# Kernel optimization log

Measured on AMD Instinct MI355X. Metric: run time of the kernel, lower is better.

Reference implementation:

```python
import jax, jax.numpy as jnp
import numpy as np

GRID_SIZE = 5
SPLINE_ORDER = 3
GRID_RANGE = (-1.0, 1.0)
LAYERS = [1024, 1024, 1024]
BATCH = 8192
LN_EPS = 1e-5


def _make_grid(in_features):
    h = (GRID_RANGE[1] - GRID_RANGE[0]) / GRID_SIZE
    n = GRID_SIZE + 2 * SPLINE_ORDER + 1  # 12 knots
    g = jnp.linspace(GRID_RANGE[0] - h * SPLINE_ORDER,
                     GRID_RANGE[1] + h * SPLINE_ORDER, n, dtype=jnp.float32)
    return jnp.broadcast_to(g, (in_features, n))


def setup_inputs() -> dict:
    key = jax.random.key(0)
    ks = jax.random.split(key, 8)
    n_layers = len(LAYERS) - 1
    d_in, d_out = LAYERS[0], LAYERS[1]  # square layers -> stackable params
    coeff = GRID_SIZE + SPLINE_ORDER  # 8
    # kaiming_uniform_(nonlinearity='linear'): bound = sqrt(3) * (1/sqrt(fan_in))
    bw_bound = float(np.sqrt(3.0) / np.sqrt(d_in))
    sw_bound = float(np.sqrt(3.0) / np.sqrt(d_in * coeff))
    x = jax.random.normal(ks[0], (BATCH, d_in), dtype=jnp.float32)
    base_w = jax.random.uniform(ks[1], (n_layers, d_out, d_in), jnp.float32, -bw_bound, bw_bound)
    spline_w = jax.random.uniform(ks[2], (n_layers, d_out, d_in, coeff), jnp.float32, -sw_bound, sw_bound)
    ln_g = jnp.ones((n_layers, d_out), jnp.float32)
    ln_b = jnp.zeros((n_layers, d_out), jnp.float32)
    prelu_a = jnp.full((n_layers,), 0.25, jnp.float32)
    grid = jnp.stack([_make_grid(d_in) for _ in range(n_layers)])  # [L, in, 12]
    return {"x": x, "base_w": base_w, "spline_w": spline_w,
            "ln_g": ln_g, "ln_b": ln_b, "prelu_a": prelu_a, "grid": grid}


def _bspline_bases(x, g):
    """Cox-de Boor recursion. x: [B, in], g: [in, n_knots] -> [B, in, G+order]."""
    xu = x[..., None]  # [B, in, 1]
    bases = ((xu >= g[:, :-1]) & (xu < g[:, 1:])).astype(x.dtype)  # [B, in, 11]
    for k in range(1, SPLINE_ORDER + 1):
        left = g[:, :-(k + 1)]
        right = g[:, k:-1]
        delta = jnp.where(right == left, jnp.ones_like(right), right - left)
        bases = ((xu - left) / delta * bases[..., :-1]
                 + (g[:, k + 1:] - xu) / (g[:, k + 1:] - g[:, 1:-k]) * bases[..., 1:])
    return bases  # [B, in, 8]


def kan_forward(x, base_w, spline_w, ln_g, ln_b, prelu_a, grid):
    n_layers = base_w.shape[0]
    for i in range(n_layers):
        base_out = jnp.matmul(jax.nn.gelu(x, approximate=False), base_w[i].T)  # [B, out]
        bases = _bspline_bases(x, grid[i])  # [B, in, 8]
        spline_out = jnp.matmul(bases.reshape(x.shape[0], -1),
                                spline_w[i].reshape(spline_w.shape[1], -1).T)  # [B, out]
        h = base_out + spline_out
        mu = jnp.mean(h, axis=-1, keepdims=True)
        var = jnp.var(h, axis=-1, keepdims=True)  # biased, matches torch LayerNorm
        h = (h - mu) * jax.lax.rsqrt(var + LN_EPS) * ln_g[i] + ln_b[i]
        x = jnp.where(h >= 0, h, prelu_a[i] * h)  # PReLU (scalar slope per layer)
    return x


def reference(x, base_w, spline_w, ln_g, ln_b, prelu_a, grid):
    return kan_forward(x, base_w, spline_w, ln_g, ln_b, prelu_a, grid)
```

## Files before the change

kernel.cpp:

```cpp
#include <hip/hip_runtime.h>
#include <hip/hip_bf16.h>
#include <cstdint>
#include <cstddef>

typedef __bf16 bf16_t;
typedef __bf16 bf16x8 __attribute__((ext_vector_type(8)));
typedef __bf16 bf16x4 __attribute__((ext_vector_type(4)));
typedef float  f32x4  __attribute__((ext_vector_type(4)));

#define DIM    1024
#define NCOEF  8
#define KTOT   (DIM + DIM * NCOEF)
#define NKNOT  12
#define BATCH  8192
#define LN_EPS 1e-5f

__device__ __forceinline__ float gelu_exact(float x) {
    return 0.5f * x * (1.0f + erff(x * 0.70710678118654752440f));
}

__global__ void pack_w(const float* __restrict__ bw, const float* __restrict__ sw,
                       bf16_t* __restrict__ W) {
    int idx = blockIdx.x * 256 + threadIdx.x;
    bf16_t* wrow = W + (size_t)(idx >> 10) * KTOT;
    int j = idx & 1023;
    wrow[j] = (bf16_t)bw[idx];
    const float4* sp = (const float4*)(sw + (size_t)idx * NCOEF);
    float4 s0 = sp[0], s1 = sp[1];
    bf16x8 v;
    v[0] = (bf16_t)s0.x; v[1] = (bf16_t)s0.y; v[2] = (bf16_t)s0.z; v[3] = (bf16_t)s0.w;
    v[4] = (bf16_t)s1.x; v[5] = (bf16_t)s1.y; v[6] = (bf16_t)s1.z; v[7] = (bf16_t)s1.w;
    *(bf16x8*)(wrow + DIM + j * NCOEF) = v;
}

__global__ void prep_gelu(const float* __restrict__ x, bf16_t* __restrict__ g) {
    int idx = blockIdx.x * 256 + threadIdx.x;
    float4 v = ((const float4*)x)[idx];
    bf16x4 o;
    o[0] = (bf16_t)gelu_exact(v.x); o[1] = (bf16_t)gelu_exact(v.y);
    o[2] = (bf16_t)gelu_exact(v.z); o[3] = (bf16_t)gelu_exact(v.w);
    *(bf16x4*)(g + (size_t)idx * 4) = o;
}

__device__ __forceinline__ void gl_lds16(const void* g, void* l) {
    __builtin_amdgcn_global_load_lds(
        (const __attribute__((address_space(1))) unsigned int*)(uintptr_t)g,
        (__attribute__((address_space(3))) unsigned int*)(uintptr_t)l, 16, 0, 0);
}

__device__ __forceinline__ uint64_t pack4bf(float a, float b, float c, float d) {
    union { bf16_t h[4]; uint64_t q; } u;
    u.h[0] = (bf16_t)a; u.h[1] = (bf16_t)b; u.h[2] = (bf16_t)c; u.h[3] = (bf16_t)d;
    return u.q;
}

__device__ __forceinline__ void spline8(float x, float g0, float invh,
                                        uint64_t& lo, uint64_t& hi) {
    float u = (x - g0) * invh;
    float jf = floorf(u);
    int j = (int)jf;
    float f = u - jf;
    float f2 = f * f, f3 = f2 * f;
    float om = 1.0f - f, om2 = om * om;
    float w0 = om2 * om * (1.0f / 6.0f);
    float w3 = f3 * (1.0f / 6.0f);
    float w1 = fmaf(0.5f, f3, 2.0f / 3.0f) - f2;
    float w2 = 1.0f - w0 - w1 - w3;
    uint64_t W64 = pack4bf(w0, w1, w2, w3);
    if (!(u >= 0.0f && u < 11.0f)) W64 = 0;
    int sh = (j - 3) * 16;
    if (sh >= 0) {
        int s = sh & 63;
        uint64_t loW = W64 << s;
        uint64_t hiW = s ? (W64 >> (64 - s)) : 0ull;
        lo = (sh < 64) ? loW : 0ull;
        hi = (sh < 64) ? hiW : loW;
    } else {
        lo = W64 >> (-sh);
        hi = 0ull;
    }
}

__device__ __forceinline__ void mfma_tile(const bf16_t* __restrict__ Ar0,
                                          const bf16_t* __restrict__ Ar1,
                                          const bf16_t* __restrict__ Br0,
                                          const bf16_t* __restrict__ Br1,
                                          f32x4 (&acc)[4][4]) {
#pragma unroll
    for (int kk = 0; kk < 2; kk++) {
        const bf16_t* Ar = kk ? Ar1 : Ar0;
        const bf16_t* Br = kk ? Br1 : Br0;
        bf16x8 af[4], bfr[4];
#pragma unroll
        for (int i = 0; i < 4; i++) af[i] = *(const bf16x8*)(Ar + i * 16 * 64);
#pragma unroll
        for (int j = 0; j < 4; j++) bfr[j] = *(const bf16x8*)(Br + j * 16 * 64);
#pragma unroll
        for (int i = 0; i < 4; i++)
#pragma unroll
            for (int j = 0; j < 4; j++)
                acc[i][j] = __builtin_amdgcn_mfma_f32_16x16x32_bf16(af[i], bfr[j], acc[i][j], 0, 0, 0);
    }
}

__global__ __launch_bounds__(256) void gemm_fused(
    const float* __restrict__ Y,
    const bf16_t* __restrict__ G,
    const bf16_t* __restrict__ W,
    float* __restrict__ C,
    const float* __restrict__ gp,
    int mmask, int mshift) {
    constexpr int K = KTOT, N = DIM;
    __shared__ __align__(16) bf16_t At[64 * 64];
    __shared__ __align__(16) bf16_t Bt[256 * 64];
    const int tid = threadIdx.x;
    const int l = tid & 63;
    const int w = tid >> 6;
    const int bm = blockIdx.x & mmask, bn = blockIdx.x >> mshift;

    const float g0 = gp[0];
    const float invh = 1.0f / (gp[1] - gp[0]);

    const int lrow = tid >> 3;
    const int lchk = (tid & 7) ^ (lrow & 7);
    const bf16_t* Gg = G + (size_t)(bm * 64 + lrow) * DIM + lchk * 8;
    const bf16_t* Bg = W + (size_t)(bn * 256 + lrow) * K + lchk * 8;
    bf16_t* Al = At + tid * 8;
    bf16_t* Bl = Bt + tid * 8;

    const float* Yb = Y + (size_t)(bm * 64 + lrow) * DIM + (tid & 7);
    bf16_t* As = At + lrow * 64 + lchk * 8;

    f32x4 acc[4][4] = {};
    const int cA = (l >> 4) ^ (l & 7);
    const bf16_t* Ar0 = At + (l & 15) * 64 + cA * 8;
    const bf16_t* Ar1 = At + (l & 15) * 64 + (cA ^ 4) * 8;
    const bf16_t* Br0 = Bt + (w * 64 + (l & 15)) * 64 + cA * 8;
    const bf16_t* Br1 = Bt + (w * 64 + (l & 15)) * 64 + (cA ^ 4) * 8;

    for (int k0 = 0; k0 < DIM; k0 += 64) {
#pragma unroll
        for (int q = 0; q < 2; q++)
            gl_lds16(Gg + (size_t)q * 32 * DIM + k0, Al + q * 2048);
#pragma unroll
        for (int q = 0; q < 8; q++)
            gl_lds16(Bg + (size_t)q * 32 * K + k0, Bl + q * 2048);
        asm volatile("s_waitcnt vmcnt(0)" ::: "memory");
        __syncthreads();
        mfma_tile(Ar0, Ar1, Br0, Br1, acc);
        __syncthreads();
    }

    float ycur[2], ynext[2];
#pragma unroll
    for (int q = 0; q < 2; q++) ycur[q] = Yb[(size_t)q * 32 * DIM];

    for (int k0 = DIM; k0 < K; k0 += 64) {
        const int j0 = (k0 - DIM) >> 3;
        const bool more = (k0 + 64) < K;
        if (more) {
#pragma unroll
            for (int q = 0; q < 2; q++) ynext[q] = Yb[(size_t)q * 32 * DIM + j0 + 8];
        }
#pragma unroll
        for (int q = 0; q < 8; q++)
            gl_lds16(Bg + (size_t)q * 32 * K + k0, Bl + q * 2048);
#pragma unroll
        for (int q = 0; q < 2; q++) {
            uint64_t lo, hi;
            spline8(ycur[q], g0, invh, lo, hi);
            union { uint64_t u[2]; uint4 v; } ov;
            ov.u[0] = lo; ov.u[1] = hi;
            *(uint4*)(As + q * 32 * 64) = ov.v;
        }
        asm volatile("s_waitcnt vmcnt(0)" ::: "memory");
        __syncthreads();
        mfma_tile(Ar0, Ar1, Br0, Br1, acc);
        __syncthreads();
        if (more) {
#pragma unroll
            for (int q = 0; q < 2; q++) ycur[q] = ynext[q];
        }
    }

    const int r0 = bm * 64 + (l >> 4) * 4;
    const int c0 = bn * 256 + w * 64 + (l & 15);
#pragma unroll
    for (int i = 0; i < 4; i++)
#pragma unroll
        for (int j = 0; j < 4; j++)
#pragma unroll
            for (int r = 0; r < 4; r++)
                C[(size_t)(r0 + i * 16 + r) * N + c0 + j * 16] = acc[i][j][r];
}

__global__ void ln_mid(const float* __restrict__ h, const float* __restrict__ g_ln,
                       const float* __restrict__ b_ln, const float* __restrict__ pa,
                       float* __restrict__ y, bf16_t* __restrict__ yg) {
    const int row = blockIdx.x, tid = threadIdx.x;
    const int w = tid >> 6, l = tid & 63;
    f32x4 v = *(const f32x4*)(h + (size_t)row * DIM + tid * 4);
    float s = v[0] + v[1] + v[2] + v[3];
    float q = v[0] * v[0] + v[1] * v[1] + v[2] * v[2] + v[3] * v[3];
#pragma unroll
    for (int o = 32; o > 0; o >>= 1) { s += __shfl_xor(s, o); q += __shfl_xor(q, o); }
    __shared__ float rs[4], rq[4];
    if (l == 0) { rs[w] = s; rq[w] = q; }
    __syncthreads();
    s = rs[0] + rs[1] + rs[2] + rs[3];
    q = rq[0] + rq[1] + rq[2] + rq[3];
    float mean = s * (1.0f / DIM);
    float var = q * (1.0f / DIM) - mean * mean;
    float rstd = rsqrtf(var + LN_EPS);
    float a = pa[0];
    f32x4 o4;
    bf16x4 g4;
#pragma unroll
    for (int c = 0; c < 4; c++) {
        int col = tid * 4 + c;
        float yv = (v[c] - mean) * rstd * g_ln[col] + b_ln[col];
        yv = (yv >= 0.0f) ? yv : a * yv;
        o4[c] = yv;
        g4[c] = (bf16_t)gelu_exact(yv);
    }
    *(f32x4*)(y + (size_t)row * DIM + tid * 4) = o4;
    *(bf16x4*)(yg + (size_t)row * DIM + tid * 4) = g4;
}

__global__ void ln_out(const float* __restrict__ h, const float* __restrict__ g_ln,
                       const float* __restrict__ b_ln, const float* __restrict__ pa,
                       float* __restrict__ out) {
    const int row = blockIdx.x, tid = threadIdx.x;
    const int w = tid >> 6, l = tid & 63;
    f32x4 v = *(const f32x4*)(h + (size_t)row * DIM + tid * 4);
    float s = v[0] + v[1] + v[2] + v[3];
    float q = v[0] * v[0] + v[1] * v[1] + v[2] * v[2] + v[3] * v[3];
#pragma unroll
    for (int o = 32; o > 0; o >>= 1) { s += __shfl_xor(s, o); q += __shfl_xor(q, o); }
    __shared__ float rs[4], rq[4];
    if (l == 0) { rs[w] = s; rq[w] = q; }
    __syncthreads();
    s = rs[0] + rs[1] + rs[2] + rs[3];
    q = rq[0] + rq[1] + rq[2] + rq[3];
    float mean = s * (1.0f / DIM);
    float var = q * (1.0f / DIM) - mean * mean;
    float rstd = rsqrtf(var + LN_EPS);
    float a = pa[0];
    f32x4 o4;
#pragma unroll
    for (int c = 0; c < 4; c++) {
        int col = tid * 4 + c;
        float yv = (v[c] - mean) * rstd * g_ln[col] + b_ln[col];
        o4[c] = (yv >= 0.0f) ? yv : a * yv;
    }
    *(f32x4*)(out + (size_t)row * DIM + tid * 4) = o4;
}

extern "C" void kernel_launch(void* const* d_in, const int* in_sizes, int n_in,
                              void* d_out, int out_size, void* d_ws, size_t ws_size,
                              hipStream_t stream) {
    const float* x    = (const float*)d_in[0];
    const float* bw   = (const float*)d_in[1];
    const float* sw   = (const float*)d_in[2];
    const float* ln_g = (const float*)d_in[3];
    const float* ln_b = (const float*)d_in[4];
    const float* pa   = (const float*)d_in[5];
    const float* grid = (const float*)d_in[6];
    float* out = (float*)d_out;

    const size_t wbytes = (size_t)2 * DIM * KTOT * sizeof(bf16_t);
    int R = 8192;
    while (R > 128 && wbytes + (size_t)R * DIM * 10 > ws_size) R >>= 1;
    int mtiles = R / 64;
    int mshift = 0; while ((1 << mshift) < mtiles) mshift++;
    int mmask = mtiles - 1;

    char* wsc = (char*)d_ws;
    bf16_t* Wbuf = (bf16_t*)wsc;
    bf16_t* ygel = (bf16_t*)(wsc + wbytes);
    float*  ybuf = (float*)(wsc + wbytes + (size_t)R * DIM * 2);
    float*  hbuf = (float*)(wsc + wbytes + (size_t)R * DIM * 6);

    pack_w<<<(2 * DIM * DIM) / 256, 256, 0, stream>>>(bw, sw, Wbuf);

    const int nslab = BATCH / R;
    for (int sidx = 0; sidx < nslab; sidx++) {
        const size_t row0 = (size_t)sidx * R;
        const float* x0 = x + row0 * DIM;
        prep_gelu<<<R * DIM / 1024, 256, 0, stream>>>(x0, ygel);
        gemm_fused<<<mtiles * 4, 256, 0, stream>>>(x0, ygel, Wbuf, hbuf,
                                                   grid, mmask, mshift);
        ln_mid<<<R, 256, 0, stream>>>(hbuf, ln_g, ln_b, pa, ybuf, ygel);
        gemm_fused<<<mtiles * 4, 256, 0, stream>>>(ybuf, ygel, Wbuf + (size_t)DIM * KTOT, hbuf,
                                                   grid + DIM * NKNOT, mmask, mshift);
        ln_out<<<R, 256, 0, stream>>>(hbuf, ln_g + DIM, ln_b + DIM, pa + 1, out + row0 * DIM);
    }
}
```

Before: 544.0 us.

## Rewrite fused KAN GEMM with 256x256 tiles, split-K, and multi-stage LDS pipeline

The GEMM kernel moves from 64x256 tiles with 256 threads to 256x256 tiles with 512 threads. K is split into two halves whose partial outputs are written to separate buffers and summed inside the LayerNorm kernels. A four-stage LDS ring now prefetches B, G and the raw activations through direct global-to-LDS loads, and the spline bases are computed into LDS while the matrix ops run. It uses s_setprio and a custom block-to-tile mapping. The aim is to raise data reuse and hide memory latency, at the cost of a large LDS footprint, extra partial-sum traffic and workspace, and a fragile hand-written schedule.

```diff
diff --git a/kernel.cpp b/kernel.cpp
--- a/kernel.cpp
+++ b/kernel.cpp
@@ -11,41 +11,25 @@
 #define DIM    1024
 #define NCOEF  8
 #define KTOT   (DIM + DIM * NCOEF)
+#define KHALF  (KTOT / 2)
+#define NT     144
 #define NKNOT  12
 #define BATCH  8192
 #define LN_EPS 1e-5f
 
 __device__ __forceinline__ float gelu_exact(float x) {
     return 0.5f * x * (1.0f + erff(x * 0.70710678118654752440f));
-}
-
-__global__ void pack_w(const float* __restrict__ bw, const float* __restrict__ sw,
-                       bf16_t* __restrict__ W) {
-    int idx = blockIdx.x * 256 + threadIdx.x;
-    bf16_t* wrow = W + (size_t)(idx >> 10) * KTOT;
-    int j = idx & 1023;
-    wrow[j] = (bf16_t)bw[idx];
-    const float4* sp = (const float4*)(sw + (size_t)idx * NCOEF);
-    float4 s0 = sp[0], s1 = sp[1];
-    bf16x8 v;
-    v[0] = (bf16_t)s0.x; v[1] = (bf16_t)s0.y; v[2] = (bf16_t)s0.z; v[3] = (bf16_t)s0.w;
-    v[4] = (bf16_t)s1.x; v[5] = (bf16_t)s1.y; v[6] = (bf16_t)s1.z; v[7] = (bf16_t)s1.w;
-    *(bf16x8*)(wrow + DIM + j * NCOEF) = v;
-}
-
-__global__ void prep_gelu(const float* __restrict__ x, bf16_t* __restrict__ g) {
-    int idx = blockIdx.x * 256 + threadIdx.x;
-    float4 v = ((const float4*)x)[idx];
-    bf16x4 o;
-    o[0] = (bf16_t)gelu_exact(v.x); o[1] = (bf16_t)gelu_exact(v.y);
-    o[2] = (bf16_t)gelu_exact(v.z); o[3] = (bf16_t)gelu_exact(v.w);
-    *(bf16x4*)(g + (size_t)idx * 4) = o;
 }
 
 __device__ __forceinline__ void gl_lds16(const void* g, void* l) {
     __builtin_amdgcn_global_load_lds(
         (const __attribute__((address_space(1))) unsigned int*)(uintptr_t)g,
         (__attribute__((address_space(3))) unsigned int*)(uintptr_t)l, 16, 0, 0);
+}
+__device__ __forceinline__ void gl_lds4(const void* g, void* l) {
+    __builtin_amdgcn_global_load_lds(
+        (const __attribute__((address_space(1))) unsigned int*)(uintptr_t)g,
+        (__attribute__((address_space(3))) unsigned int*)(uintptr_t)l, 4, 0, 0);
 }
 
 __device__ __forceinline__ uint64_t pack4bf(float a, float b, float c, float d) {
@@ -81,125 +65,199 @@
     }
 }
 
-__device__ __forceinline__ void mfma_tile(const bf16_t* __restrict__ Ar0,
-                                          const bf16_t* __restrict__ Ar1,
-                                          const bf16_t* __restrict__ Br0,
-                                          const bf16_t* __restrict__ Br1,
-                                          f32x4 (&acc)[4][4]) {
-#pragma unroll
-    for (int kk = 0; kk < 2; kk++) {
-        const bf16_t* Ar = kk ? Ar1 : Ar0;
-        const bf16_t* Br = kk ? Br1 : Br0;
-        bf16x8 af[4], bfr[4];
-#pragma unroll
-        for (int i = 0; i < 4; i++) af[i] = *(const bf16x8*)(Ar + i * 16 * 64);
-#pragma unroll
-        for (int j = 0; j < 4; j++) bfr[j] = *(const bf16x8*)(Br + j * 16 * 64);
-#pragma unroll
-        for (int i = 0; i < 4; i++)
-#pragma unroll
-            for (int j = 0; j < 4; j++)
-                acc[i][j] = __builtin_amdgcn_mfma_f32_16x16x32_bf16(af[i], bfr[j], acc[i][j], 0, 0, 0);
-    }
-}
-
-__global__ __launch_bounds__(256) void gemm_fused(
+__global__ void pack_w(const float* __restrict__ bw, const float* __restrict__ sw,
+                       bf16_t* __restrict__ W) {
+    int idx = blockIdx.x * 256 + threadIdx.x;
+    bf16_t* wrow = W + (size_t)(idx >> 10) * KTOT;
+    int j = idx & 1023;
+    wrow[j] = (bf16_t)bw[idx];
+    const float4* sp = (const float4*)(sw + (size_t)idx * NCOEF);
+    float4 s0 = sp[0], s1 = sp[1];
+    bf16x8 v;
+    v[0] = (bf16_t)s0.x; v[1] = (bf16_t)s0.y; v[2] = (bf16_t)s0.z; v[3] = (bf16_t)s0.w;
+    v[4] = (bf16_t)s1.x; v[5] = (bf16_t)s1.y; v[6] = (bf16_t)s1.z; v[7] = (bf16_t)s1.w;
+    *(bf16x8*)(wrow + DIM + j * NCOEF) = v;
+}
+
+__global__ void prep_gelu(const float* __restrict__ x, bf16_t* __restrict__ g) {
+    int idx = blockIdx.x * 256 + threadIdx.x;
+    float4 v = ((const float4*)x)[idx];
+    bf16x4 o;
+    o[0] = (bf16_t)gelu_exact(v.x); o[1] = (bf16_t)gelu_exact(v.y);
+    o[2] = (bf16_t)gelu_exact(v.z); o[3] = (bf16_t)gelu_exact(v.w);
+    *(bf16x4*)(g + (size_t)idx * 4) = o;
+}
+
+
+#define STAGE_B(U, S) \
+    gl_lds16(BgA + (size_t)(U) * 32, ldsb + 32768 + (S) * 8192 + tid * 8); \
+    gl_lds16(BgB + (size_t)(U) * 32, ldsb + 32768 + (S) * 8192 + 4096 + tid * 8);
+
+#define STAGE_G(U, S) \
+    gl_lds16(GgA + (size_t)(U) * 32, ldsb + (S) * 8192 + tid * 8); \
+    gl_lds16(GgB + (size_t)(U) * 32, ldsb + (S) * 8192 + 4096 + tid * 8);
+
+#define STAGE_Y(U, S) { int jb_ = jb0 + (U) * 4; \
+    gl_lds4(YgA + jb_, ldsy + (S) * 1024 + tid); \
+    gl_lds4(YgB + jb_, ldsy + (S) * 1024 + 512 + tid); }
+
+#define COMPUTE_A(S) { \
+    float x1_ = ldsy[(S) * 1024 + tid], x2_ = ldsy[(S) * 1024 + 512 + tid]; \
+    uint64_t lo_, hi_; union { uint64_t u[2]; uint4 v; } ov_; \
+    spline8(x1_, g0, invh, lo_, hi_); ov_.u[0] = lo_; ov_.u[1] = hi_; \
+    *(uint4*)(ldsb + (S) * 8192 + tid * 8) = ov_.v; \
+    spline8(x2_, g0, invh, lo_, hi_); ov_.u[0] = lo_; ov_.u[1] = hi_; \
+    *(uint4*)(ldsb + (S) * 8192 + 4096 + tid * 8) = ov_.v; }
+
+#define RD_B(S) { const bf16_t* Bb_ = ldsb + 32768 + (S) * 8192 + bOff; \
+    b0 = *(const bf16x8*)(Bb_);        b1 = *(const bf16x8*)(Bb_ + 512); \
+    b2 = *(const bf16x8*)(Bb_ + 1024); b3 = *(const bf16x8*)(Bb_ + 1536); }
+
+#define MF_ROW(I, A_) \
+    acc[I][0] = __builtin_amdgcn_mfma_f32_16x16x32_bf16(A_, b0, acc[I][0], 0, 0, 0); \
+    acc[I][1] = __builtin_amdgcn_mfma_f32_16x16x32_bf16(A_, b1, acc[I][1], 0, 0, 0); \
+    acc[I][2] = __builtin_amdgcn_mfma_f32_16x16x32_bf16(A_, b2, acc[I][2], 0, 0, 0); \
+    acc[I][3] = __builtin_amdgcn_mfma_f32_16x16x32_bf16(A_, b3, acc[I][3], 0, 0, 0);
+
+#define MF_HALF(S, IB) { const bf16_t* Ab_ = ldsb + (S) * 8192 + aOff + (IB) * 2048; \
+    bf16x8 a0_ = *(const bf16x8*)(Ab_),        a1_ = *(const bf16x8*)(Ab_ + 512), \
+           a2_ = *(const bf16x8*)(Ab_ + 1024), a3_ = *(const bf16x8*)(Ab_ + 1536); \
+    __builtin_amdgcn_s_setprio(1); \
+    MF_ROW((IB) * 4 + 0, a0_) MF_ROW((IB) * 4 + 1, a1_) \
+    MF_ROW((IB) * 4 + 2, a2_) MF_ROW((IB) * 4 + 3, a3_) \
+    __builtin_amdgcn_s_setprio(0); }
+
+#define ITER(T, SA0, SA1, SS0, SS1) { \
+    const int u2_ = 2 * (T) + 2, u3_ = 2 * (T) + 3; \
+    bf16x8 b0, b1, b2, b3; \
+     \
+    if (u2_ < NT) { STAGE_B(u2_, SS0) } \
+    if ((T) < 70) { asm volatile("s_waitcnt vmcnt(6)" ::: "memory"); } \
+    else          { asm volatile("s_waitcnt vmcnt(0)" ::: "memory"); } \
+    __builtin_amdgcn_s_barrier(); \
+    asm volatile("" ::: "memory"); \
+    RD_B(SA0) \
+    MF_HALF(SA0, 0) \
+    __builtin_amdgcn_s_barrier(); \
+     \
+    if (u2_ + 2 < NT && (koff0 + (u2_ + 2) * 32) >= DIM) { STAGE_Y(u2_ + 2, SA0) } \
+    if (u2_ < NT) { \
+        if (koff0 + u2_ * 32 < DIM) { STAGE_G(u2_, SS0) } \
+        else                        { COMPUTE_A(SS0) } \
+    } \
+    MF_HALF(SA0, 1) \
+     \
+    if (u3_ < NT) { STAGE_B(u3_, SS1) } \
+    if ((T) < 70) { asm volatile("s_waitcnt vmcnt(6)" ::: "memory"); } \
+    else          { asm volatile("s_waitcnt vmcnt(0)" ::: "memory"); } \
+    __builtin_amdgcn_s_barrier(); \
+    asm volatile("" ::: "memory"); \
+    RD_B(SA1) \
+    MF_HALF(SA1, 0) \
+    __builtin_amdgcn_s_barrier(); \
+     \
+    if (u3_ + 2 < NT && (koff0 + (u3_ + 2) * 32) >= DIM) { STAGE_Y(u3_ + 2, SA1) } \
+    if (u3_ < NT) { \
+        if (koff0 + u3_ * 32 < DIM) { STAGE_G(u3_, SS1) } \
+        else                        { COMPUTE_A(SS1) } \
+    } \
+    MF_HALF(SA1, 1) \
+    asm volatile("s_waitcnt lgkmcnt(0)" ::: "memory"); \
+    __builtin_amdgcn_s_barrier(); \
+}
+
+__global__ __launch_bounds__(512, 2) void gemm_fused(
     const float* __restrict__ Y,
     const bf16_t* __restrict__ G,
     const bf16_t* __restrict__ W,
     float* __restrict__ C,
     const float* __restrict__ gp,
-    int mmask, int mshift) {
-    constexpr int K = KTOT, N = DIM;
-    __shared__ __align__(16) bf16_t At[64 * 64];
-    __shared__ __align__(16) bf16_t Bt[256 * 64];
+    int mmask, int mshift, int rows) {
+    __shared__ __align__(16) unsigned char smem[147456];
+    bf16_t* __restrict__ ldsb = (bf16_t*)smem;
+    float*  __restrict__ ldsy = (float*)(smem + 131072);
+
     const int tid = threadIdx.x;
-    const int l = tid & 63;
-    const int w = tid >> 6;
-    const int bm = blockIdx.x & mmask, bn = blockIdx.x >> mshift;
+    const int l = tid & 63, wv = tid >> 6;
+    const int wm = wv >> 2, wn = wv & 3;
+
+    const int chunk = mmask + 1;
+    const int bid = blockIdx.x;
+    const int wg = (bid & 7) * chunk + (bid >> 3);
+    const int bm = wg & mmask;
+    const int bn = (wg >> mshift) & 3;
+    const int ks = wg >> (mshift + 2);
+    const int row0 = bm << 8;
+    const int col0 = bn << 8;
+    const int koff0 = ks * KHALF;
+    const int jb0 = (koff0 >> 3) - 128;
 
     const float g0 = gp[0];
     const float invh = 1.0f / (gp[1] - gp[0]);
 
-    const int lrow = tid >> 3;
-    const int lchk = (tid & 7) ^ (lrow & 7);
-    const bf16_t* Gg = G + (size_t)(bm * 64 + lrow) * DIM + lchk * 8;
-    const bf16_t* Bg = W + (size_t)(bn * 256 + lrow) * K + lchk * 8;
-    bf16_t* Al = At + tid * 8;
-    bf16_t* Bl = Bt + tid * 8;
-
-    const float* Yb = Y + (size_t)(bm * 64 + lrow) * DIM + (tid & 7);
-    bf16_t* As = At + lrow * 64 + lchk * 8;
-
-    f32x4 acc[4][4] = {};
-    const int cA = (l >> 4) ^ (l & 7);
-    const bf16_t* Ar0 = At + (l & 15) * 64 + cA * 8;
-    const bf16_t* Ar1 = At + (l & 15) * 64 + (cA ^ 4) * 8;
-    const bf16_t* Br0 = Bt + (w * 64 + (l & 15)) * 64 + cA * 8;
-    const bf16_t* Br1 = Bt + (w * 64 + (l & 15)) * 64 + (cA ^ 4) * 8;
-
-    for (int k0 = 0; k0 < DIM; k0 += 64) {
-#pragma unroll
-        for (int q = 0; q < 2; q++)
-            gl_lds16(Gg + (size_t)q * 32 * DIM + k0, Al + q * 2048);
-#pragma unroll
-        for (int q = 0; q < 8; q++)
-            gl_lds16(Bg + (size_t)q * 32 * K + k0, Bl + q * 2048);
+    const int srow = tid >> 2;
+    const int slc  = (tid & 3) ^ ((srow >> 1) & 3);
+    const bf16_t* __restrict__ BgA = W + (size_t)(col0 + srow) * KTOT + koff0 + slc * 8;
+    const bf16_t* __restrict__ BgB = BgA + (size_t)128 * KTOT;
+    const bf16_t* __restrict__ GgA = G + (size_t)(row0 + srow) * DIM + slc * 8;
+    const bf16_t* __restrict__ GgB = GgA + (size_t)128 * DIM;
+    const float*  __restrict__ YgA = Y + (size_t)(row0 + srow) * DIM + slc;
+    const float*  __restrict__ YgB = YgA + (size_t)128 * DIM;
+
+    const int l15 = l & 15;
+    const int pc = (l >> 4) ^ ((l15 >> 1) & 3);
+    const int aOff = (wm * 128 + l15) * 32 + pc * 8;
+    const int bOff = (wn * 64 + l15) * 32 + pc * 8;
+
+    f32x4 acc[8][4] = {};
+
+    STAGE_B(0, 0)
+    STAGE_B(1, 1)
+    if (koff0 == 0) {
+        STAGE_G(0, 0)
+        STAGE_G(1, 1)
         asm volatile("s_waitcnt vmcnt(0)" ::: "memory");
-        __syncthreads();
-        mfma_tile(Ar0, Ar1, Br0, Br1, acc);
-        __syncthreads();
-    }
-
-    float ycur[2], ynext[2];
-#pragma unroll
-    for (int q = 0; q < 2; q++) ycur[q] = Yb[(size_t)q * 32 * DIM];
-
-    for (int k0 = DIM; k0 < K; k0 += 64) {
-        const int j0 = (k0 - DIM) >> 3;
-        const bool more = (k0 + 64) < K;
-        if (more) {
-#pragma unroll
-            for (int q = 0; q < 2; q++) ynext[q] = Yb[(size_t)q * 32 * DIM + j0 + 8];
-        }
-#pragma unroll
-        for (int q = 0; q < 8; q++)
-            gl_lds16(Bg + (size_t)q * 32 * K + k0, Bl + q * 2048);
-#pragma unroll
-        for (int q = 0; q < 2; q++) {
-            uint64_t lo, hi;
-            spline8(ycur[q], g0, invh, lo, hi);
-            union { uint64_t u[2]; uint4 v; } ov;
-            ov.u[0] = lo; ov.u[1] = hi;
-            *(uint4*)(As + q * 32 * 64) = ov.v;
-        }
+        __builtin_amdgcn_s_barrier();
+        asm volatile("" ::: "memory");
+    } else {
+        STAGE_Y(0, 0) STAGE_Y(1, 1) STAGE_Y(2, 2) STAGE_Y(3, 3)
         asm volatile("s_waitcnt vmcnt(0)" ::: "memory");
-        __syncthreads();
-        mfma_tile(Ar0, Ar1, Br0, Br1, acc);
-        __syncthreads();
-        if (more) {
-#pragma unroll
-            for (int q = 0; q < 2; q++) ycur[q] = ynext[q];
-        }
-    }
-
-    const int r0 = bm * 64 + (l >> 4) * 4;
-    const int c0 = bn * 256 + w * 64 + (l & 15);
-#pragma unroll
-    for (int i = 0; i < 4; i++)
+        __builtin_amdgcn_s_barrier();
+        asm volatile("" ::: "memory");
+        COMPUTE_A(0)
+        COMPUTE_A(1)
+        asm volatile("s_waitcnt lgkmcnt(0)" ::: "memory");
+        __builtin_amdgcn_s_barrier();
+        asm volatile("" ::: "memory");
+    }
+
+#pragma unroll 1
+    for (int t = 0; t < 72; t += 2) {
+        ITER(t,     0, 1, 2, 3)
+        ITER(t + 1, 2, 3, 0, 1)
+    }
+
+    float* __restrict__ Cp = C + (size_t)ks * rows * DIM;
+    const int r0 = row0 + wm * 128 + (l >> 4) * 4;
+    const int c0 = col0 + wn * 64 + l15;
+#pragma unroll
+    for (int i = 0; i < 8; i++)
 #pragma unroll
         for (int j = 0; j < 4; j++)
 #pragma unroll
             for (int r = 0; r < 4; r++)
-                C[(size_t)(r0 + i * 16 + r) * N + c0 + j * 16] = acc[i][j][r];
-}
-
-__global__ void ln_mid(const float* __restrict__ h, const float* __restrict__ g_ln,
-                       const float* __restrict__ b_ln, const float* __restrict__ pa,
+                Cp[(size_t)(r0 + i * 16 + r) * DIM + c0 + j * 16] = acc[i][j][r];
+}
+
+__global__ void ln_mid(const float* __restrict__ ha, const float* __restrict__ hb,
+                       const float* __restrict__ g_ln, const float* __restrict__ b_ln,
+                       const float* __restrict__ pa,
                        float* __restrict__ y, bf16_t* __restrict__ yg) {
     const int row = blockIdx.x, tid = threadIdx.x;
     const int w = tid >> 6, l = tid & 63;
-    f32x4 v = *(const f32x4*)(h + (size_t)row * DIM + tid * 4);
+    f32x4 va = *(const f32x4*)(ha + (size_t)row * DIM + tid * 4);
+    f32x4 vb = *(const f32x4*)(hb + (size_t)row * DIM + tid * 4);
+    f32x4 v = va + vb;
     float s = v[0] + v[1] + v[2] + v[3];
     float q = v[0] * v[0] + v[1] * v[1] + v[2] * v[2] + v[3] * v[3];
 #pragma unroll
@@ -227,12 +285,14 @@
     *(bf16x4*)(yg + (size_t)row * DIM + tid * 4) = g4;
 }
 
-__global__ void ln_out(const float* __restrict__ h, const float* __restrict__ g_ln,
-                       const float* __restrict__ b_ln, const float* __restrict__ pa,
-                       float* __restrict__ out) {
+__global__ void ln_out(const float* __restrict__ ha, const float* __restrict__ hb,
+                       const float* __restrict__ g_ln, const float* __restrict__ b_ln,
+                       const float* __restrict__ pa, float* __restrict__ out) {
     const int row = blockIdx.x, tid = threadIdx.x;
     const int w = tid >> 6, l = tid & 63;
-    f32x4 v = *(const f32x4*)(h + (size_t)row * DIM + tid * 4);
+    f32x4 va = *(const f32x4*)(ha + (size_t)row * DIM + tid * 4);
+    f32x4 vb = *(const f32x4*)(hb + (size_t)row * DIM + tid * 4);
+    f32x4 v = va + vb;
     float s = v[0] + v[1] + v[2] + v[3];
     float q = v[0] * v[0] + v[1] * v[1] + v[2] * v[2] + v[3] * v[3];
 #pragma unroll
@@ -265,15 +325,16 @@
     const float* ln_g = (const float*)d_in[3];
     const float* ln_b = (const float*)d_in[4];
     const float* pa   = (const float*)d_in[5];
-    const float* grid = (const float*)d_in[6];
+    const float* gridK = (const float*)d_in[6];
     float* out = (float*)d_out;
 
     const size_t wbytes = (size_t)2 * DIM * KTOT * sizeof(bf16_t);
     int R = 8192;
-    while (R > 128 && wbytes + (size_t)R * DIM * 10 > ws_size) R >>= 1;
-    int mtiles = R / 64;
+    while (R > 256 && wbytes + (size_t)R * DIM * 14 > ws_size) R >>= 1;
+    int mtiles = R / 256;
     int mshift = 0; while ((1 << mshift) < mtiles) mshift++;
     int mmask = mtiles - 1;
+    int grid = mtiles * 8;
 
     char* wsc = (char*)d_ws;
     bf16_t* Wbuf = (bf16_t*)wsc;
@@ -288,11 +349,13 @@
         const size_t row0 = (size_t)sidx * R;
         const float* x0 = x + row0 * DIM;
         prep_gelu<<<R * DIM / 1024, 256, 0, stream>>>(x0, ygel);
-        gemm_fused<<<mtiles * 4, 256, 0, stream>>>(x0, ygel, Wbuf, hbuf,
-                                                   grid, mmask, mshift);
-        ln_mid<<<R, 256, 0, stream>>>(hbuf, ln_g, ln_b, pa, ybuf, ygel);
-        gemm_fused<<<mtiles * 4, 256, 0, stream>>>(ybuf, ygel, Wbuf + (size_t)DIM * KTOT, hbuf,
-                                                   grid + DIM * NKNOT, mmask, mshift);
-        ln_out<<<R, 256, 0, stream>>>(hbuf, ln_g + DIM, ln_b + DIM, pa + 1, out + row0 * DIM);
-    }
-}
+        gemm_fused<<<grid, 512, 0, stream>>>(x0, ygel, Wbuf, hbuf,
+                                             gridK, mmask, mshift, R);
+        ln_mid<<<R, 256, 0, stream>>>(hbuf, hbuf + (size_t)R * DIM,
+                                      ln_g, ln_b, pa, ybuf, ygel);
+        gemm_fused<<<grid, 512, 0, stream>>>(ybuf, ygel, Wbuf + (size_t)DIM * KTOT, hbuf,
+                                             gridK + DIM * NKNOT, mmask, mshift, R);
+        ln_out<<<R, 256, 0, stream>>>(hbuf, hbuf + (size_t)R * DIM,
+                                      ln_g + DIM, ln_b + DIM, pa + 1, out + row0 * DIM);
+    }
+}
```

Result: no change. 544.4 us (+0.1%).

## Materialize spline bases in A matrix and use split-K pipelined 256x256 GEMM

Applied to the files above, without the earlier changes.

The B-spline basis expansion moves out of the GEMM inner loop. Prep and LayerNorm kernels now write a full bf16 A matrix holding GELU values plus 8 spline coefficients per input. The GEMM is rewritten with 256x256 tiles, 512 threads, a 4-stage global-to-LDS pipeline, setprio around the MFMA work, and split-K with partial sums that the LayerNorm kernels reduce. This trades extra HBM traffic for the materialized A and the partial outputs against much higher MFMA utilization and better data reuse.

```diff
diff --git a/kernel.cpp b/kernel.cpp
--- a/kernel.cpp
+++ b/kernel.cpp
@@ -17,29 +17,6 @@
 
 __device__ __forceinline__ float gelu_exact(float x) {
     return 0.5f * x * (1.0f + erff(x * 0.70710678118654752440f));
-}
-
-__global__ void pack_w(const float* __restrict__ bw, const float* __restrict__ sw,
-                       bf16_t* __restrict__ W) {
-    int idx = blockIdx.x * 256 + threadIdx.x;
-    bf16_t* wrow = W + (size_t)(idx >> 10) * KTOT;
-    int j = idx & 1023;
-    wrow[j] = (bf16_t)bw[idx];
-    const float4* sp = (const float4*)(sw + (size_t)idx * NCOEF);
-    float4 s0 = sp[0], s1 = sp[1];
-    bf16x8 v;
-    v[0] = (bf16_t)s0.x; v[1] = (bf16_t)s0.y; v[2] = (bf16_t)s0.z; v[3] = (bf16_t)s0.w;
-    v[4] = (bf16_t)s1.x; v[5] = (bf16_t)s1.y; v[6] = (bf16_t)s1.z; v[7] = (bf16_t)s1.w;
-    *(bf16x8*)(wrow + DIM + j * NCOEF) = v;
-}
-
-__global__ void prep_gelu(const float* __restrict__ x, bf16_t* __restrict__ g) {
-    int idx = blockIdx.x * 256 + threadIdx.x;
-    float4 v = ((const float4*)x)[idx];
-    bf16x4 o;
-    o[0] = (bf16_t)gelu_exact(v.x); o[1] = (bf16_t)gelu_exact(v.y);
-    o[2] = (bf16_t)gelu_exact(v.z); o[3] = (bf16_t)gelu_exact(v.w);
-    *(bf16x4*)(g + (size_t)idx * 4) = o;
 }
 
 __device__ __forceinline__ void gl_lds16(const void* g, void* l) {
@@ -81,125 +58,195 @@
     }
 }
 
-__device__ __forceinline__ void mfma_tile(const bf16_t* __restrict__ Ar0,
-                                          const bf16_t* __restrict__ Ar1,
-                                          const bf16_t* __restrict__ Br0,
-                                          const bf16_t* __restrict__ Br1,
-                                          f32x4 (&acc)[4][4]) {
-#pragma unroll
-    for (int kk = 0; kk < 2; kk++) {
-        const bf16_t* Ar = kk ? Ar1 : Ar0;
-        const bf16_t* Br = kk ? Br1 : Br0;
-        bf16x8 af[4], bfr[4];
-#pragma unroll
-        for (int i = 0; i < 4; i++) af[i] = *(const bf16x8*)(Ar + i * 16 * 64);
-#pragma unroll
-        for (int j = 0; j < 4; j++) bfr[j] = *(const bf16x8*)(Br + j * 16 * 64);
-#pragma unroll
-        for (int i = 0; i < 4; i++)
-#pragma unroll
-            for (int j = 0; j < 4; j++)
-                acc[i][j] = __builtin_amdgcn_mfma_f32_16x16x32_bf16(af[i], bfr[j], acc[i][j], 0, 0, 0);
-    }
-}
-
-__global__ __launch_bounds__(256) void gemm_fused(
-    const float* __restrict__ Y,
-    const bf16_t* __restrict__ G,
+__global__ void pack_w(const float* __restrict__ bw, const float* __restrict__ sw,
+                       bf16_t* __restrict__ W) {
+    int idx = blockIdx.x * 256 + threadIdx.x;
+    bf16_t* wrow = W + (size_t)(idx >> 10) * KTOT;
+    int j = idx & 1023;
+    wrow[j] = (bf16_t)bw[idx];
+    const float4* sp = (const float4*)(sw + (size_t)idx * NCOEF);
+    float4 s0 = sp[0], s1 = sp[1];
+    bf16x8 v;
+    v[0] = (bf16_t)s0.x; v[1] = (bf16_t)s0.y; v[2] = (bf16_t)s0.z; v[3] = (bf16_t)s0.w;
+    v[4] = (bf16_t)s1.x; v[5] = (bf16_t)s1.y; v[6] = (bf16_t)s1.z; v[7] = (bf16_t)s1.w;
+    *(bf16x8*)(wrow + DIM + j * NCOEF) = v;
+}
+
+__global__ void prep_A(const float* __restrict__ x, bf16_t* __restrict__ A,
+                       const float* __restrict__ gp) {
+    const int row = blockIdx.x, t = threadIdx.x;
+    const float g0 = gp[0];
+    const float invh = 1.0f / (gp[1] - gp[0]);
+    f32x4 v = *(const f32x4*)(x + (size_t)row * DIM + t * 4);
+    bf16_t* Ar = A + (size_t)row * KTOT;
+    bf16x4 ge;
+#pragma unroll
+    for (int k = 0; k < 4; k++) ge[k] = (bf16_t)gelu_exact(v[k]);
+    *(bf16x4*)(Ar + t * 4) = ge;
+#pragma unroll
+    for (int k = 0; k < 4; k++) {
+        uint64_t lo, hi;
+        union { uint64_t u[2]; uint4 q; } o;
+        spline8(v[k], g0, invh, lo, hi);
+        o.u[0] = lo; o.u[1] = hi;
+        *(uint4*)(Ar + DIM + (t * 4 + k) * NCOEF) = o.q;
+    }
+}
+
+
+#define STAGE(T, S) { \
+    const size_t ko_ = (size_t)(T) * 32; \
+    gl_lds16(Ag0 + ko_, ldsA + (S) * 8192 + tid * 8); \
+    gl_lds16(Ag1 + ko_, ldsA + (S) * 8192 + 4096 + tid * 8); \
+    gl_lds16(Bg0 + ko_, ldsB + (S) * 8192 + tid * 8); \
+    gl_lds16(Bg1 + ko_, ldsB + (S) * 8192 + 4096 + tid * 8); }
+
+#define MF_ROW(I, A_) \
+    acc[I][0] = __builtin_amdgcn_mfma_f32_16x16x32_bf16(A_, b0_, acc[I][0], 0, 0, 0); \
+    acc[I][1] = __builtin_amdgcn_mfma_f32_16x16x32_bf16(A_, b1_, acc[I][1], 0, 0, 0); \
+    acc[I][2] = __builtin_amdgcn_mfma_f32_16x16x32_bf16(A_, b2_, acc[I][2], 0, 0, 0); \
+    acc[I][3] = __builtin_amdgcn_mfma_f32_16x16x32_bf16(A_, b3_, acc[I][3], 0, 0, 0);
+
+#define TILE_COMPUTE(S) { \
+    const bf16_t* Bb_ = ldsB + (S) * 8192 + bOff; \
+    bf16x8 b0_ = *(const bf16x8*)(Bb_),        b1_ = *(const bf16x8*)(Bb_ + 512), \
+           b2_ = *(const bf16x8*)(Bb_ + 1024), b3_ = *(const bf16x8*)(Bb_ + 1536); \
+    const bf16_t* Ab_ = ldsA + (S) * 8192 + aOff; \
+    { bf16x8 a0_ = *(const bf16x8*)(Ab_),        a1_ = *(const bf16x8*)(Ab_ + 512), \
+             a2_ = *(const bf16x8*)(Ab_ + 1024), a3_ = *(const bf16x8*)(Ab_ + 1536); \
+      __builtin_amdgcn_s_setprio(1); \
+      MF_ROW(0, a0_) MF_ROW(1, a1_) MF_ROW(2, a2_) MF_ROW(3, a3_) \
+      __builtin_amdgcn_s_setprio(0); } \
+    { bf16x8 a4_ = *(const bf16x8*)(Ab_ + 2048), a5_ = *(const bf16x8*)(Ab_ + 2560), \
+             a6_ = *(const bf16x8*)(Ab_ + 3072), a7_ = *(const bf16x8*)(Ab_ + 3584); \
+      __builtin_amdgcn_s_setprio(1); \
+      MF_ROW(4, a4_) MF_ROW(5, a5_) MF_ROW(6, a6_) MF_ROW(7, a7_) \
+      __builtin_amdgcn_s_setprio(0); } }
+
+#define BAR() { __builtin_amdgcn_s_barrier(); asm volatile("" ::: "memory"); }
+
+#define TILE_MAIN(T, S, SP) { \
+    STAGE((T) + 2, SP) \
+    asm volatile("s_waitcnt vmcnt(8)" ::: "memory"); \
+    BAR() \
+    TILE_COMPUTE(S) }
+
+template<int NTK>
+__global__ __launch_bounds__(512, 2) void gemm_ab(
+    const bf16_t* __restrict__ A,
     const bf16_t* __restrict__ W,
     float* __restrict__ C,
-    const float* __restrict__ gp,
-    int mmask, int mshift) {
-    constexpr int K = KTOT, N = DIM;
-    __shared__ __align__(16) bf16_t At[64 * 64];
-    __shared__ __align__(16) bf16_t Bt[256 * 64];
+    int mmask, int mshift, int rows) {
+    __shared__ __align__(16) bf16_t lds[65536];
+    bf16_t* __restrict__ ldsA = lds;
+    bf16_t* __restrict__ ldsB = lds + 32768;
+
     const int tid = threadIdx.x;
-    const int l = tid & 63;
-    const int w = tid >> 6;
-    const int bm = blockIdx.x & mmask, bn = blockIdx.x >> mshift;
-
+    const int l = tid & 63, wv = tid >> 6;
+    const int wm = wv >> 2, wn = wv & 3;
+
+    const int chunk = gridDim.x >> 3;
+    const int bid = blockIdx.x;
+    const int wg = (bid & 7) * chunk + (bid >> 3);
+    const int bm = wg & mmask;
+    const int bn = (wg >> mshift) & 3;
+    const int ks = wg >> (mshift + 2);
+    const int row0 = bm << 8, col0 = bn << 8;
+    const int koff0 = ks * (NTK * 32);
+
+    const int srow = tid >> 2;
+    const int slc = (tid & 3) ^ ((srow >> 1) & 3);
+    const bf16_t* __restrict__ Ag0 = A + (size_t)(row0 + srow) * KTOT + koff0 + slc * 8;
+    const bf16_t* __restrict__ Ag1 = Ag0 + (size_t)128 * KTOT;
+    const bf16_t* __restrict__ Bg0 = W + (size_t)(col0 + srow) * KTOT + koff0 + slc * 8;
+    const bf16_t* __restrict__ Bg1 = Bg0 + (size_t)128 * KTOT;
+
+    const int l15 = l & 15;
+    const int pc = (l >> 4) ^ ((l15 >> 1) & 3);
+    const int aOff = (wm * 128 + l15) * 32 + pc * 8;
+    const int bOff = (wn * 64 + l15) * 32 + pc * 8;
+
+    f32x4 acc[8][4] = {};
+
+    STAGE(0, 0)
+    STAGE(1, 1)
+#pragma unroll 1
+    for (int t = 0; t < NTK - 4; t += 4) {
+        TILE_MAIN(t,     0, 2)
+        TILE_MAIN(t + 1, 1, 3)
+        TILE_MAIN(t + 2, 2, 0)
+        TILE_MAIN(t + 3, 3, 1)
+    }
+    TILE_MAIN(NTK - 4, 0, 2)
+    TILE_MAIN(NTK - 3, 1, 3)
+    asm volatile("s_waitcnt vmcnt(4)" ::: "memory");
+    BAR()
+    TILE_COMPUTE(2)
+    asm volatile("s_waitcnt vmcnt(0)" ::: "memory");
+    BAR()
+    TILE_COMPUTE(3)
+
+    float* __restrict__ Cp = C + (size_t)ks * rows * DIM;
+    const int r0 = row0 + wm * 128 + (l >> 4) * 4;
+    const int c0 = col0 + wn * 64 + l15;
+#pragma unroll
+    for (int i = 0; i < 8; i++)
+#pragma unroll
+        for (int j = 0; j < 4; j++)
+#pragma unroll
+            for (int r = 0; r < 4; r++)
+                Cp[(size_t)(r0 + i * 16 + r) * DIM + c0 + j * 16] = acc[i][j][r];
+}
+
+__global__ void ln_mid_A(const float* __restrict__ h, int rows, int ksplit,
+                         const float* __restrict__ g_ln, const float* __restrict__ b_ln,
+                         const float* __restrict__ pa, bf16_t* __restrict__ A,
+                         const float* __restrict__ gp) {
+    const int row = blockIdx.x, tid = threadIdx.x;
+    const int w = tid >> 6, l = tid & 63;
+    f32x4 v = {0.0f, 0.0f, 0.0f, 0.0f};
+    for (int ks = 0; ks < ksplit; ks++)
+        v += *(const f32x4*)(h + ((size_t)ks * rows + row) * DIM + tid * 4);
+    float s = v[0] + v[1] + v[2] + v[3];
+    float q = v[0] * v[0] + v[1] * v[1] + v[2] * v[2] + v[3] * v[3];
+#pragma unroll
+    for (int o = 32; o > 0; o >>= 1) { s += __shfl_xor(s, o); q += __shfl_xor(q, o); }
+    __shared__ float rs[4], rq[4];
+    if (l == 0) { rs[w] = s; rq[w] = q; }
+    __syncthreads();
+    s = rs[0] + rs[1] + rs[2] + rs[3];
+    q = rq[0] + rq[1] + rq[2] + rq[3];
+    float mean = s * (1.0f / DIM);
+    float var = q * (1.0f / DIM) - mean * mean;
+    float rstd = rsqrtf(var + LN_EPS);
+    float a = pa[0];
     const float g0 = gp[0];
     const float invh = 1.0f / (gp[1] - gp[0]);
-
-    const int lrow = tid >> 3;
-    const int lchk = (tid & 7) ^ (lrow & 7);
-    const bf16_t* Gg = G + (size_t)(bm * 64 + lrow) * DIM + lchk * 8;
-    const bf16_t* Bg = W + (size_t)(bn * 256 + lrow) * K + lchk * 8;
-    bf16_t* Al = At + tid * 8;
-    bf16_t* Bl = Bt + tid * 8;
-
-    const float* Yb = Y + (size_t)(bm * 64 + lrow) * DIM + (tid & 7);
-    bf16_t* As = At + lrow * 64 + lchk * 8;
-
-    f32x4 acc[4][4] = {};
-    const int cA = (l >> 4) ^ (l & 7);
-    const bf16_t* Ar0 = At + (l & 15) * 64 + cA * 8;
-    const bf16_t* Ar1 = At + (l & 15) * 64 + (cA ^ 4) * 8;
-    const bf16_t* Br0 = Bt + (w * 64 + (l & 15)) * 64 + cA * 8;
-    const bf16_t* Br1 = Bt + (w * 64 + (l & 15)) * 64 + (cA ^ 4) * 8;
-
-    for (int k0 = 0; k0 < DIM; k0 += 64) {
-#pragma unroll
-        for (int q = 0; q < 2; q++)
-            gl_lds16(Gg + (size_t)q * 32 * DIM + k0, Al + q * 2048);
-#pragma unroll
-        for (int q = 0; q < 8; q++)
-            gl_lds16(Bg + (size_t)q * 32 * K + k0, Bl + q * 2048);
-        asm volatile("s_waitcnt vmcnt(0)" ::: "memory");
-        __syncthreads();
-        mfma_tile(Ar0, Ar1, Br0, Br1, acc);
-        __syncthreads();
-    }
-
-    float ycur[2], ynext[2];
-#pragma unroll
-    for (int q = 0; q < 2; q++) ycur[q] = Yb[(size_t)q * 32 * DIM];
-
-    for (int k0 = DIM; k0 < K; k0 += 64) {
-        const int j0 = (k0 - DIM) >> 3;
-        const bool more = (k0 + 64) < K;
-        if (more) {
-#pragma unroll
-            for (int q = 0; q < 2; q++) ynext[q] = Yb[(size_t)q * 32 * DIM + j0 + 8];
-        }
-#pragma unroll
-        for (int q = 0; q < 8; q++)
-            gl_lds16(Bg + (size_t)q * 32 * K + k0, Bl + q * 2048);
-#pragma unroll
-        for (int q = 0; q < 2; q++) {
-            uint64_t lo, hi;
-            spline8(ycur[q], g0, invh, lo, hi);
-            union { uint64_t u[2]; uint4 v; } ov;
-            ov.u[0] = lo; ov.u[1] = hi;
-            *(uint4*)(As + q * 32 * 64) = ov.v;
-        }
-        asm volatile("s_waitcnt vmcnt(0)" ::: "memory");
-        __syncthreads();
-        mfma_tile(Ar0, Ar1, Br0, Br1, acc);
-        __syncthreads();
-        if (more) {
-#pragma unroll
-            for (int q = 0; q < 2; q++) ycur[q] = ynext[q];
-        }
-    }
-
-    const int r0 = bm * 64 + (l >> 4) * 4;
-    const int c0 = bn * 256 + w * 64 + (l & 15);
-#pragma unroll
-    for (int i = 0; i < 4; i++)
-#pragma unroll
-        for (int j = 0; j < 4; j++)
-#pragma unroll
-            for (int r = 0; r < 4; r++)
-                C[(size_t)(r0 + i * 16 + r) * N + c0 + j * 16] = acc[i][j][r];
-}
-
-__global__ void ln_mid(const float* __restrict__ h, const float* __restrict__ g_ln,
-                       const float* __restrict__ b_ln, const float* __restrict__ pa,
-                       float* __restrict__ y, bf16_t* __restrict__ yg) {
+    bf16_t* Ar = A + (size_t)row * KTOT;
+    bf16x4 ge;
+#pragma unroll
+    for (int c = 0; c < 4; c++) {
+        int col = tid * 4 + c;
+        float yv = (v[c] - mean) * rstd * g_ln[col] + b_ln[col];
+        yv = (yv >= 0.0f) ? yv : a * yv;
+        ge[c] = (bf16_t)gelu_exact(yv);
+        uint64_t lo, hi;
+        union { uint64_t u[2]; uint4 qv; } o;
+        spline8(yv, g0, invh, lo, hi);
+        o.u[0] = lo; o.u[1] = hi;
+        *(uint4*)(Ar + DIM + (size_t)col * NCOEF) = o.qv;
+    }
+    *(bf16x4*)(Ar + tid * 4) = ge;
+}
+
+__global__ void ln_out(const float* __restrict__ h, int rows, int ksplit,
+                       const float* __restrict__ g_ln, const float* __restrict__ b_ln,
+                       const float* __restrict__ pa, float* __restrict__ out) {
     const int row = blockIdx.x, tid = threadIdx.x;
     const int w = tid >> 6, l = tid & 63;
-    f32x4 v = *(const f32x4*)(h + (size_t)row * DIM + tid * 4);
+    f32x4 v = {0.0f, 0.0f, 0.0f, 0.0f};
+    for (int ks = 0; ks < ksplit; ks++)
+        v += *(const f32x4*)(h + ((size_t)ks * rows + row) * DIM + tid * 4);
     float s = v[0] + v[1] + v[2] + v[3];
     float q = v[0] * v[0] + v[1] * v[1] + v[2] * v[2] + v[3] * v[3];
 #pragma unroll
@@ -214,39 +261,6 @@
     float rstd = rsqrtf(var + LN_EPS);
     float a = pa[0];
     f32x4 o4;
-    bf16x4 g4;
-#pragma unroll
-    for (int c = 0; c < 4; c++) {
-        int col = tid * 4 + c;
-        float yv = (v[c] - mean) * rstd * g_ln[col] + b_ln[col];
-        yv = (yv >= 0.0f) ? yv : a * yv;
-        o4[c] = yv;
-        g4[c] = (bf16_t)gelu_exact(yv);
-    }
-    *(f32x4*)(y + (size_t)row * DIM + tid * 4) = o4;
-    *(bf16x4*)(yg + (size_t)row * DIM + tid * 4) = g4;
-}
-
-__global__ void ln_out(const float* __restrict__ h, const float* __restrict__ g_ln,
-                       const float* __restrict__ b_ln, const float* __restrict__ pa,
-                       float* __restrict__ out) {
-    const int row = blockIdx.x, tid = threadIdx.x;
-    const int w = tid >> 6, l = tid & 63;
-    f32x4 v = *(const f32x4*)(h + (size_t)row * DIM + tid * 4);
-    float s = v[0] + v[1] + v[2] + v[3];
-    float q = v[0] * v[0] + v[1] * v[1] + v[2] * v[2] + v[3] * v[3];
-#pragma unroll
-    for (int o = 32; o > 0; o >>= 1) { s += __shfl_xor(s, o); q += __shfl_xor(q, o); }
-    __shared__ float rs[4], rq[4];
-    if (l == 0) { rs[w] = s; rq[w] = q; }
-    __syncthreads();
-    s = rs[0] + rs[1] + rs[2] + rs[3];
-    q = rq[0] + rq[1] + rq[2] + rq[3];
-    float mean = s * (1.0f / DIM);
-    float var = q * (1.0f / DIM) - mean * mean;
-    float rstd = rsqrtf(var + LN_EPS);
-    float a = pa[0];
-    f32x4 o4;
 #pragma unroll
     for (int c = 0; c < 4; c++) {
         int col = tid * 4 + c;
@@ -265,34 +279,49 @@
     const float* ln_g = (const float*)d_in[3];
     const float* ln_b = (const float*)d_in[4];
     const float* pa   = (const float*)d_in[5];
-    const float* grid = (const float*)d_in[6];
+    const float* gridK = (const float*)d_in[6];
     float* out = (float*)d_out;
 
     const size_t wbytes = (size_t)2 * DIM * KTOT * sizeof(bf16_t);
-    int R = 8192;
-    while (R > 128 && wbytes + (size_t)R * DIM * 10 > ws_size) R >>= 1;
-    int mtiles = R / 64;
+    int R = 8192, ksplit = 2;
+    for (;;) {
+        size_t need = wbytes + (size_t)R * KTOT * 2 + (size_t)ksplit * R * DIM * 4;
+        if (need <= ws_size || R == 512) break;
+        R >>= 1;
+        int mt = R / 256;
+        ksplit = (mt >= 32) ? 2 : (mt >= 16) ? 4 : 8;
+    }
+    int mtiles = R / 256;
     int mshift = 0; while ((1 << mshift) < mtiles) mshift++;
     int mmask = mtiles - 1;
+    int grid = mtiles * 4 * ksplit;
 
     char* wsc = (char*)d_ws;
     bf16_t* Wbuf = (bf16_t*)wsc;
-    bf16_t* ygel = (bf16_t*)(wsc + wbytes);
-    float*  ybuf = (float*)(wsc + wbytes + (size_t)R * DIM * 2);
-    float*  hbuf = (float*)(wsc + wbytes + (size_t)R * DIM * 6);
+    bf16_t* Abuf = (bf16_t*)(wsc + wbytes);
+    float*  hbuf = (float*)(wsc + wbytes + (size_t)R * KTOT * 2);
 
     pack_w<<<(2 * DIM * DIM) / 256, 256, 0, stream>>>(bw, sw, Wbuf);
+
+    auto launch_gemm = [&](const bf16_t* Wl, hipStream_t st) {
+        if (ksplit == 2)
+            gemm_ab<144><<<grid, 512, 0, st>>>(Abuf, Wl, hbuf, mmask, mshift, R);
+        else if (ksplit == 4)
+            gemm_ab<72><<<grid, 512, 0, st>>>(Abuf, Wl, hbuf, mmask, mshift, R);
+        else
+            gemm_ab<36><<<grid, 512, 0, st>>>(Abuf, Wl, hbuf, mmask, mshift, R);
+    };
 
     const int nslab = BATCH / R;
     for (int sidx = 0; sidx < nslab; sidx++) {
         const size_t row0 = (size_t)sidx * R;
         const float* x0 = x + row0 * DIM;
-        prep_gelu<<<R * DIM / 1024, 256, 0, stream>>>(x0, ygel);
-        gemm_fused<<<mtiles * 4, 256, 0, stream>>>(x0, ygel, Wbuf, hbuf,
-                                                   grid, mmask, mshift);
-        ln_mid<<<R, 256, 0, stream>>>(hbuf, ln_g, ln_b, pa, ybuf, ygel);
-        gemm_fused<<<mtiles * 4, 256, 0, stream>>>(ybuf, ygel, Wbuf + (size_t)DIM * KTOT, hbuf,
-                                                   grid + DIM * NKNOT, mmask, mshift);
-        ln_out<<<R, 256, 0, stream>>>(hbuf, ln_g + DIM, ln_b + DIM, pa + 1, out + row0 * DIM);
-    }
-}
+        prep_A<<<R, 256, 0, stream>>>(x0, Abuf, gridK);
+        launch_gemm(Wbuf, stream);
+        ln_mid_A<<<R, 256, 0, stream>>>(hbuf, R, ksplit, ln_g, ln_b, pa,
+                                        Abuf, gridK + DIM * NKNOT);
+        launch_gemm(Wbuf + (size_t)DIM * KTOT, stream);
+        ln_out<<<R, 256, 0, stream>>>(hbuf, R, ksplit, ln_g + DIM, ln_b + DIM,
+                                      pa + 1, out + row0 * DIM);
+    }
+}
```

Result: slower. 574.1 us (+5.5%).
